# Optimization experiments

Measured on AMD Instinct MI355X. Metric: run time of the kernel, lower is better.

## Reference

```python
import jax, jax.numpy as jnp
import numpy as np

D_MODEL = 1024
NHEAD = 16
EPS = 1e-5


def pos_embed(x, pos):
    # Faithful, vectorized form of the sparse rotation matrix in the source.
    # Source builds rot[..., i, i+1] = sin(pos*i*omega) for even i and
    # rot[..., i, i-1] = cos(pos*i*omega) for odd i, then contracts the feature
    # dim of x against the rotation (intended einsum 'btf,btfd->btd').
    # Resulting column j: even j <- x[..., j+1]*cos(pos*(j+1)*omega),
    #                     odd  j <- x[..., j-1]*sin(pos*(j-1)*omega).
    d = x.shape[-1]
    omega = jnp.pi / d
    i_even = jnp.arange(0, d, 2, dtype=x.dtype)   # even rows -> odd output cols (sin)
    i_odd = jnp.arange(1, d, 2, dtype=x.dtype)    # odd rows  -> even output cols (cos)
    p = pos[..., None]  # (L,B,1)
    sin_part = jnp.sin(p * i_even * omega) * x[..., 0::2]  # -> odd columns
    cos_part = jnp.cos(p * i_odd * omega) * x[..., 1::2]   # -> even columns
    # interleave: even col = cos_part, odd col = sin_part
    return jnp.stack([cos_part, sin_part], axis=-1).reshape(x.shape)


def layer_norm_eps(x, w, b):
    # Source uses torch.var default (unbiased, ddof=1)
    mean = jnp.mean(x, axis=-1, keepdims=True)
    var = jnp.var(x, axis=-1, keepdims=True, ddof=1)
    return w * (x - mean) / jnp.sqrt(var + EPS) + b


def mha(q, k, v, w_qkv, b_qkv, w_o, b_o, nhead):
    L, B, E = q.shape
    S = k.shape[0]
    hd = E // nhead
    wq, wk, wv = jnp.split(w_qkv, 3, axis=0)
    bq, bk, bv = jnp.split(b_qkv, 3, axis=0)
    qp = (q @ wq.T + bq).reshape(L, B, nhead, hd).transpose(1, 2, 0, 3)  # (B,h,L,hd)
    kp = (k @ wk.T + bk).reshape(S, B, nhead, hd).transpose(1, 2, 0, 3)
    vp = (v @ wv.T + bv).reshape(S, B, nhead, hd).transpose(1, 2, 0, 3)
    scale = jnp.asarray(1.0 / np.sqrt(hd), q.dtype)
    scores = jnp.einsum('bhld,bhsd->bhls', qp, kp) * scale
    attn = jax.nn.softmax(scores, axis=-1)
    out = jnp.einsum('bhls,bhsd->bhld', attn, vp)
    out = out.transpose(2, 0, 1, 3).reshape(L, B, E) @ w_o.T + b_o
    ws = attn.mean(axis=1)  # average over heads, torch default
    return out, ws


def setup_inputs() -> dict:
    key = jax.random.key(0)
    ks = jax.random.split(key, 16)
    T, S, B, E, FF = 1024, 1024, 4, D_MODEL, 4096
    sd = 0.02
    return {
        'tgt': jax.random.normal(ks[0], (T, B, E), jnp.float32),
        'memory': jax.random.normal(ks[1], (S, B, E), jnp.float32),
        'pos': jax.random.uniform(ks[2], (S, B), jnp.float32) * S,
        'query_pos': jax.random.uniform(ks[3], (T, B), jnp.float32) * T,
        'w_qkv_self': jax.random.normal(ks[4], (3 * E, E), jnp.float32) * sd,
        'b_qkv_self': jnp.zeros((3 * E,), jnp.float32),
        'w_o_self': jax.random.normal(ks[5], (E, E), jnp.float32) * sd,
        'b_o_self': jnp.zeros((E,), jnp.float32),
        'w_qkv_cross': jax.random.normal(ks[6], (3 * E, E), jnp.float32) * sd,
        'b_qkv_cross': jnp.zeros((3 * E,), jnp.float32),
        'w_o_cross': jax.random.normal(ks[7], (E, E), jnp.float32) * sd,
        'b_o_cross': jnp.zeros((E,), jnp.float32),
        'w1': jax.random.normal(ks[8], (FF, E), jnp.float32) * sd,
        'b1': jnp.zeros((FF,), jnp.float32),
        'w2': jax.random.normal(ks[9], (E, FF), jnp.float32) * sd,
        'b2': jnp.zeros((E,), jnp.float32),
        'g1': jnp.ones((E,), jnp.float32),
        'beta1': jnp.zeros((E,), jnp.float32),
        'g2': jnp.ones((E,), jnp.float32),
        'beta2': jnp.zeros((E,), jnp.float32),
    }


def reference(tgt, memory, pos, query_pos,
              w_qkv_self, b_qkv_self, w_o_self, b_o_self,
              w_qkv_cross, b_qkv_cross, w_o_cross, b_o_cross,
              w1, b1, w2, b2, g1, beta1, g2, beta2):
    # normalize_before=False, residual=True, dropout inactive (eval)
    qk = pos_embed(tgt, query_pos)
    tgt2, _ = mha(qk, qk, tgt, w_qkv_self, b_qkv_self, w_o_self, b_o_self, NHEAD)
    tgt = tgt + tgt2
    tgt = layer_norm_eps(tgt, g1, beta1)
    tgt2, ws = mha(pos_embed(tgt, query_pos), pos_embed(memory, pos), memory,
                   w_qkv_cross, b_qkv_cross, w_o_cross, b_o_cross, NHEAD)
    tgt = tgt + tgt2
    tgt = layer_norm_eps(tgt, g2, beta2)
    tgt2 = jax.nn.relu(tgt @ w1.T + b1) @ w2.T + b2
    tgt = tgt + tgt2
    return tgt, ws
```

## Files before the change

kernel.cpp:

```cpp
#include <hip/hip_runtime.h>

typedef unsigned short u16;
typedef __attribute__((ext_vector_type(8))) short short8;
typedef __attribute__((ext_vector_type(8))) unsigned short u16x8;
typedef __attribute__((ext_vector_type(4))) float f32x4;

#define GLOAD16(SRC, DST) __builtin_amdgcn_global_load_lds( \
    (const __attribute__((address_space(1))) void*)(SRC),   \
    (__attribute__((address_space(3))) void*)(DST), 16, 0, 0)

#define SWZ(BKv, r) ((BKv) == 32 ? (((r) >> 1) & 3) : ((r) & 7))

#define QSCALE 0.18033688011112042f

__device__ __forceinline__ u16 f2bf(float f) {
  union { float f; unsigned u; } v; v.f = f;
  unsigned r = v.u + 0x7fffu + ((v.u >> 16) & 1u);
  return (u16)(r >> 16);
}
__device__ __forceinline__ float bf2f(u16 h) {
  union { unsigned u; float f; } v; v.u = ((unsigned)h) << 16;
  return v.f;
}

__global__ __launch_bounds__(256) void wcvt_kernel(const float* __restrict__ s0,
                                                   const float* __restrict__ s1,
                                                   const float* __restrict__ s2,
                                                   const float* __restrict__ s3,
                                                   const float* __restrict__ s4,
                                                   const float* __restrict__ s5,
                                                   u16* __restrict__ dst) {
  long i = ((long)blockIdx.x * 256 + threadIdx.x) * 4;
  const float* src; long off;
  if (i < 3145728)        { src = s0; off = 0; }
  else if (i < 4194304)   { src = s1; off = 3145728; }
  else if (i < 7340032)   { src = s2; off = 4194304; }
  else if (i < 8388608)   { src = s3; off = 7340032; }
  else if (i < 12582912)  { src = s4; off = 8388608; }
  else                    { src = s5; off = 12582912; }
  float4 v = *(const float4*)(src + (i - off));
  ushort4 o; o.x = f2bf(v.x); o.y = f2bf(v.y); o.z = f2bf(v.z); o.w = f2bf(v.w);
  *(ushort4*)(dst + i) = o;
}

__global__ __launch_bounds__(256) void pos_embed_kernel(const float* __restrict__ x,
                                                        const float* __restrict__ pos,
                                                        u16* __restrict__ out,
                                                        u16* __restrict__ out2,
                                                        u16* __restrict__ raw) {
  int m = blockIdx.x;
  int tid = threadIdx.x;
  float p = pos[m];
  long base = ((long)m << 10);
  int j = tid * 4;
  float4 xv = *(const float4*)(x + base + j);
  const float inv = 1.0f / 2048.0f;
  float r0 = p * (float)(j + 0) * inv;
  float r1 = p * (float)(j + 1) * inv;
  float r2 = p * (float)(j + 2) * inv;
  float r3 = p * (float)(j + 3) * inv;
  float s1 = __builtin_amdgcn_sinf(r0 - floorf(r0));
  float c0 = __builtin_amdgcn_cosf(r1 - floorf(r1));
  float s3 = __builtin_amdgcn_sinf(r2 - floorf(r2));
  float c2 = __builtin_amdgcn_cosf(r3 - floorf(r3));
  ushort4 o;
  o.x = f2bf(c0 * xv.y);
  o.y = f2bf(s1 * xv.x);
  o.z = f2bf(c2 * xv.w);
  o.w = f2bf(s3 * xv.z);
  *(ushort4*)(out + base + j) = o;
  if (out2) *(ushort4*)(out2 + base + j) = o;
  if (raw) {
    ushort4 rw; rw.x = f2bf(xv.x); rw.y = f2bf(xv.y); rw.z = f2bf(xv.z); rw.w = f2bf(xv.w);
    *(ushort4*)(raw + base + j) = rw;
  }
}

__global__ __launch_bounds__(256) void fattn_kernel(const u16* __restrict__ Q,
                                                    const u16* __restrict__ K,
                                                    const u16* __restrict__ Vt,
                                                    u16* __restrict__ AO,
                                                    float2* __restrict__ Ml) {
  __shared__ u16 lK[2][4096];
  __shared__ u16 lV[2][4096];
  __shared__ u16 lP[8][1024];
  const int tid = threadIdx.x, lane = tid & 63, wid = tid >> 6;
  const int nb = gridDim.x * gridDim.y;
  const int orig = blockIdx.y * gridDim.x + blockIdx.x;
  const int swz = (orig & 7) * (nb >> 3) + (orig >> 3);
  const int qt = swz & 7;
  const int bh = swz >> 3;
  const int b = bh >> 4, h = bh & 15;
  const u16* Qp = Q + ((long)bh << 16);
  const u16* Kp = K + ((long)bh << 16);
  const u16* Vp = Vt + ((long)bh << 16);
  const int q0 = qt << 7;
  const int cr = lane >> 4;

  short8 aAf0, aAf1, aBf0, aBf1;
  {
    const u16* qs = Qp + (long)(q0 + wid * 16 + (lane & 15)) * 64 + cr * 8;
    aAf0 = *(const short8*)qs;
    aAf1 = *(const short8*)(qs + 32);
    aBf0 = *(const short8*)(qs + 4096);
    aBf1 = *(const short8*)(qs + 4096 + 32);
  }

  float mA = -1e30f, lA_ = 0.f, mB = -1e30f, lB_ = 0.f;
  f32x4 accA[4] = {}, accB[4] = {};

  auto stage = [&](int bufi, int kv) {
    int s0 = kv << 6;
#pragma unroll
    for (int it = 0; it < 2; it++) {
      int c = it * 256 + tid;
      int row = c >> 3, ch = c & 7;
      int sch = (ch ^ (row & 7)) * 8;
      GLOAD16(Kp + (long)(s0 + row) * 64 + sch, &lK[bufi][c * 8]);
      GLOAD16(Vp + (long)row * 1024 + s0 + sch, &lV[bufi][c * 8]);
    }
  };

  stage(0, 0);
  __syncthreads();
  int buf = 0;
  for (int kv = 0; kv < 16; kv++) {
    if (kv < 15) stage(buf ^ 1, kv + 1);
    f32x4 sA[4], sB[4];
    __builtin_amdgcn_s_setprio(1);
#pragma unroll
    for (int j = 0; j < 4; j++) {
      int sr = j * 16 + (lane & 15);
      const short8 kf0 = *(const short8*)&lK[buf][sr * 64 + ((cr ^ (sr & 7)) * 8)];
      const short8 kf1 = *(const short8*)&lK[buf][sr * 64 + (((4 + cr) ^ (sr & 7)) * 8)];
      f32x4 zA = {}, zB = {};
      zA = __builtin_amdgcn_mfma_f32_16x16x32_bf16(kf0, aAf0, zA, 0, 0, 0);
      zB = __builtin_amdgcn_mfma_f32_16x16x32_bf16(kf0, aBf0, zB, 0, 0, 0);
      sA[j] = __builtin_amdgcn_mfma_f32_16x16x32_bf16(kf1, aAf1, zA, 0, 0, 0);
      sB[j] = __builtin_amdgcn_mfma_f32_16x16x32_bf16(kf1, aBf1, zB, 0, 0, 0);
    }
    __builtin_amdgcn_s_setprio(0);
    {
      float tm = fmaxf(fmaxf(fmaxf(sA[0][0], sA[0][1]), fmaxf(sA[0][2], sA[0][3])),
                       fmaxf(fmaxf(sA[1][0], sA[1][1]), fmaxf(sA[1][2], sA[1][3])));
      float t2 = fmaxf(fmaxf(fmaxf(sA[2][0], sA[2][1]), fmaxf(sA[2][2], sA[2][3])),
                       fmaxf(fmaxf(sA[3][0], sA[3][1]), fmaxf(sA[3][2], sA[3][3])));
      tm = fmaxf(tm, t2);
      tm = fmaxf(tm, __shfl_xor(tm, 16));
      tm = fmaxf(tm, __shfl_xor(tm, 32));
      if (!__all(tm - mA <= 8.0f)) {
        float mn = fmaxf(mA, tm);
        float f = __builtin_amdgcn_exp2f(mA - mn);
        mA = mn; lA_ *= f;
#pragma unroll
        for (int r = 0; r < 4; r++) {
          float fr = __shfl(f, cr * 4 + r);
          accA[0][r] *= fr; accA[1][r] *= fr; accA[2][r] *= fr; accA[3][r] *= fr;
        }
      }
      float rs = 0.f;
#pragma unroll
      for (int j = 0; j < 4; j++)
#pragma unroll
        for (int r = 0; r < 4; r++) {
          float p = __builtin_amdgcn_exp2f(sA[j][r] - mA);
          sA[j][r] = p;
          rs += p;
        }
      rs += __shfl_xor(rs, 16);
      rs += __shfl_xor(rs, 32);
      lA_ += rs;
    }
    {
      float tm = fmaxf(fmaxf(fmaxf(sB[0][0], sB[0][1]), fmaxf(sB[0][2], sB[0][3])),
                       fmaxf(fmaxf(sB[1][0], sB[1][1]), fmaxf(sB[1][2], sB[1][3])));
      float t2 = fmaxf(fmaxf(fmaxf(sB[2][0], sB[2][1]), fmaxf(sB[2][2], sB[2][3])),
                       fmaxf(fmaxf(sB[3][0], sB[3][1]), fmaxf(sB[3][2], sB[3][3])));
      tm = fmaxf(tm, t2);
      tm = fmaxf(tm, __shfl_xor(tm, 16));
      tm = fmaxf(tm, __shfl_xor(tm, 32));
      if (!__all(tm - mB <= 8.0f)) {
        float mn = fmaxf(mB, tm);
        float f = __builtin_amdgcn_exp2f(mB - mn);
        mB = mn; lB_ *= f;
#pragma unroll
        for (int r = 0; r < 4; r++) {
          float fr = __shfl(f, cr * 4 + r);
          accB[0][r] *= fr; accB[1][r] *= fr; accB[2][r] *= fr; accB[3][r] *= fr;
        }
      }
      float rs = 0.f;
#pragma unroll
      for (int j = 0; j < 4; j++)
#pragma unroll
        for (int r = 0; r < 4; r++) {
          float p = __builtin_amdgcn_exp2f(sB[j][r] - mB);
          sB[j][r] = p;
          rs += p;
        }
      rs += __shfl_xor(rs, 16);
      rs += __shfl_xor(rs, 32);
      lB_ += rs;
    }
    {
      int q = lane & 15;
      int rowoff = q * 64;
      int qs7 = q & 7;
      u16* pwA = lP[wid];
      u16* pwB = lP[4 + wid];
#pragma unroll
      for (int j = 0; j < 4; j++) {
        int chunk = 2 * j + (cr >> 1);
        int idx = rowoff + ((chunk ^ qs7) * 8) + 4 * (cr & 1);
        uint2 pkA, pkB;
        asm("v_cvt_pk_bf16_f32 %0, %1, %2"
            : "=v"(pkA.x) : "v"(sA[j][0]), "v"(sA[j][1]));
        asm("v_cvt_pk_bf16_f32 %0, %1, %2"
            : "=v"(pkA.y) : "v"(sA[j][2]), "v"(sA[j][3]));
        asm("v_cvt_pk_bf16_f32 %0, %1, %2"
            : "=v"(pkB.x) : "v"(sB[j][0]), "v"(sB[j][1]));
        asm("v_cvt_pk_bf16_f32 %0, %1, %2"
            : "=v"(pkB.y) : "v"(sB[j][2]), "v"(sB[j][3]));
        *(uint2*)(pwA + idx) = pkA;
        *(uint2*)(pwB + idx) = pkB;
      }
    }
    {
      int ql = lane & 15;
      const u16* prA = &lP[wid][ql * 64];
      const u16* prB = &lP[4 + wid][ql * 64];
      short8 paA0 = *(const short8*)&prA[(cr ^ (ql & 7)) * 8];
      short8 paA1 = *(const short8*)&prA[((4 + cr) ^ (ql & 7)) * 8];
      short8 paB0 = *(const short8*)&prB[(cr ^ (ql & 7)) * 8];
      short8 paB1 = *(const short8*)&prB[((4 + cr) ^ (ql & 7)) * 8];
      __builtin_amdgcn_s_setprio(1);
#pragma unroll
      for (int j = 0; j < 4; j++) {
        int dr = j * 16 + (lane & 15);
        const short8 vf0 = *(const short8*)&lV[buf][dr * 64 + ((cr ^ (dr & 7)) * 8)];
        const short8 vf1 = *(const short8*)&lV[buf][dr * 64 + (((4 + cr) ^ (dr & 7)) * 8)];
        accA[j] = __builtin_amdgcn_mfma_f32_16x16x32_bf16(paA0, vf0, accA[j], 0, 0, 0);
        accB[j] = __builtin_amdgcn_mfma_f32_16x16x32_bf16(paB0, vf0, accB[j], 0, 0, 0);
        accA[j] = __builtin_amdgcn_mfma_f32_16x16x32_bf16(paA1, vf1, accA[j], 0, 0, 0);
        accB[j] = __builtin_amdgcn_mfma_f32_16x16x32_bf16(paB1, vf1, accB[j], 0, 0, 0);
      }
      __builtin_amdgcn_s_setprio(0);
    }
    __syncthreads();
    buf ^= 1;
  }
  float invA = 1.0f / lA_, invB = 1.0f / lB_;
  float iA[4], iB[4];
#pragma unroll
  for (int r = 0; r < 4; r++) {
    iA[r] = __shfl(invA, cr * 4 + r);
    iB[r] = __shfl(invB, cr * 4 + r);
  }
  const int ecol = (b << 10) + (h << 6);
#pragma unroll
  for (int j = 0; j < 4; j++)
#pragma unroll
    for (int r = 0; r < 4; r++) {
      int t = q0 + wid * 16 + cr * 4 + r;
      int e = ecol + j * 16 + (lane & 15);
      AO[(long)t * 4096 + e] = f2bf(accA[j][r] * iA[r]);
      AO[(long)(t + 64) * 4096 + e] = f2bf(accB[j][r] * iB[r]);
    }
  if (Ml && lane < 16) {
    int t = q0 + wid * 16 + lane;
    Ml[((long)bh << 10) + t] = make_float2(mA, invA);
    Ml[((long)bh << 10) + t + 64] = make_float2(mB, invB);
  }
}

__global__ __launch_bounds__(256) void wsrec_kernel(const u16* __restrict__ Q,
                                                    const u16* __restrict__ K,
                                                    const float2* __restrict__ Ml,
                                                    float* __restrict__ ws) {
  __shared__ u16 lK[2][4096];
  const int tid = threadIdx.x, lane = tid & 63, wid = tid >> 6;
  const int nb = gridDim.x * gridDim.y;
  const int orig = blockIdx.y * gridDim.x + blockIdx.x;
  const int swz = (orig & 7) * (nb >> 3) + (orig >> 3);
  const int st = swz & 15, lt = swz >> 4;
  const int b = blockIdx.z;
  const int s0 = st << 6, l0 = lt << 6;
  const int cr = lane >> 4;

  auto stage = [&](int bufi, int h) {
    const u16* Kp = K + (((long)(b * 16 + h)) << 16);
#pragma unroll
    for (int it = 0; it < 2; it++) {
      int c = it * 256 + tid;
      int row = c >> 3, ch = c & 7;
      GLOAD16(Kp + (long)(s0 + row) * 64 + ((ch ^ (row & 7)) * 8), &lK[bufi][c * 8]);
    }
  };

  f32x4 wacc[4] = {};
  stage(0, 0);
  __syncthreads();
  int buf = 0;
  for (int h = 0; h < 16; h++) {
    if (h < 15) stage(buf ^ 1, h + 1);
    const int bh = b * 16 + h;
    short8 af0, af1;
    {
      const u16* qs = Q + ((long)bh << 16) + (long)(l0 + wid * 16 + (lane & 15)) * 64 + cr * 8;
      af0 = *(const short8*)qs;
      af1 = *(const short8*)(qs + 32);
    }
    f32x4 accs[4];
    __builtin_amdgcn_s_setprio(1);
#pragma unroll
    for (int j = 0; j < 4; j++) {
      int sr = j * 16 + (lane & 15);
      const short8 kf0 = *(const short8*)&lK[buf][sr * 64 + ((cr ^ (sr & 7)) * 8)];
      const short8 kf1 = *(const short8*)&lK[buf][sr * 64 + (((4 + cr) ^ (sr & 7)) * 8)];
      f32x4 zz = {};
      zz = __builtin_amdgcn_mfma_f32_16x16x32_bf16(af0, kf0, zz, 0, 0, 0);
      accs[j] = __builtin_amdgcn_mfma_f32_16x16x32_bf16(af1, kf1, zz, 0, 0, 0);
    }
    __builtin_amdgcn_s_setprio(0);
    float mm[4], il[4];
#pragma unroll
    for (int r = 0; r < 4; r++) {
      float2 v = Ml[((long)bh << 10) + l0 + wid * 16 + (lane >> 4) * 4 + r];
      mm[r] = v.x; il[r] = v.y * 0.0625f;
    }
#pragma unroll
    for (int j = 0; j < 4; j++)
#pragma unroll
      for (int r = 0; r < 4; r++)
        wacc[j][r] += __builtin_amdgcn_exp2f(accs[j][r] - mm[r]) * il[r];
    __syncthreads();
    buf ^= 1;
  }
#pragma unroll
  for (int j = 0; j < 4; j++)
#pragma unroll
    for (int r = 0; r < 4; r++) {
      int li = l0 + wid * 16 + (lane >> 4) * 4 + r;
      int si = s0 + j * 16 + (lane & 15);
      ws[((long)b << 20) + (long)li * 1024 + si] = wacc[j][r];
    }
}

__global__ __launch_bounds__(256) void ln_kernel(const float* __restrict__ X,
                                                 const float* __restrict__ D1,
                                                 const float* __restrict__ D2,
                                                 const float* __restrict__ bo,
                                                 const float* __restrict__ g,
                                                 const float* __restrict__ be,
                                                 float* __restrict__ out,
                                                 u16* __restrict__ bfout,
                                                 const float* __restrict__ pepos) {
  int mrow = blockIdx.x;
  int tid = threadIdx.x, lane = tid & 63, wid = tid >> 6;
  long base = ((long)mrow << 10);
  float4 a = *(const float4*)(X + base + tid * 4);
  float4 b = *(const float4*)(D1 + base + tid * 4);
  float x0 = a.x + b.x, x1 = a.y + b.y, x2 = a.z + b.z, x3 = a.w + b.w;
  if (D2) {
    float4 c = *(const float4*)(D2 + base + tid * 4);
    x0 += c.x; x1 += c.y; x2 += c.z; x3 += c.w;
  }
  if (bo) {
    float4 c = *(const float4*)(bo + tid * 4);
    x0 += c.x; x1 += c.y; x2 += c.z; x3 += c.w;
  }
  float s = x0 + x1 + x2 + x3;
#pragma unroll
  for (int o = 32; o; o >>= 1) s += __shfl_xor(s, o);
  __shared__ float red[4];
  if (lane == 0) red[wid] = s;
  __syncthreads();
  float mean = (red[0] + red[1] + red[2] + red[3]) * (1.0f / 1024.0f);
  float d0 = x0 - mean, d1 = x1 - mean, d2 = x2 - mean, d3 = x3 - mean;
  float ss = d0 * d0 + d1 * d1 + d2 * d2 + d3 * d3;
#pragma unroll
  for (int o = 32; o; o >>= 1) ss += __shfl_xor(ss, o);
  __syncthreads();
  if (lane == 0) red[wid] = ss;
  __syncthreads();
  float var = (red[0] + red[1] + red[2] + red[3]) * (1.0f / 1023.0f);
  float sc = 1.0f / sqrtf(var + 1e-5f);
  float4 gv = *(const float4*)(g + tid * 4);
  float4 bv = *(const float4*)(be + tid * 4);
  float y0 = gv.x * d0 * sc + bv.x;
  float y1 = gv.y * d1 * sc + bv.y;
  float y2 = gv.z * d2 * sc + bv.z;
  float y3 = gv.w * d3 * sc + bv.w;
  float4 o4; o4.x = y0; o4.y = y1; o4.z = y2; o4.w = y3;
  *(float4*)(out + base + tid * 4) = o4;
  if (bfout) {
    ushort4 hh;
    if (pepos) {
      float p = pepos[mrow];
      int j = tid * 4;
      const float inv = 1.0f / 2048.0f;
      float r0 = p * (float)(j + 0) * inv;
      float r1 = p * (float)(j + 1) * inv;
      float r2 = p * (float)(j + 2) * inv;
      float r3 = p * (float)(j + 3) * inv;
      float s1 = __builtin_amdgcn_sinf(r0 - floorf(r0));
      float c0 = __builtin_amdgcn_cosf(r1 - floorf(r1));
      float s3 = __builtin_amdgcn_sinf(r2 - floorf(r2));
      float c2 = __builtin_amdgcn_cosf(r3 - floorf(r3));
      hh.x = f2bf(c0 * y1);
      hh.y = f2bf(s1 * y0);
      hh.z = f2bf(c2 * y3);
      hh.w = f2bf(s3 * y2);
    } else {
      hh.x = f2bf(y0); hh.y = f2bf(y1); hh.z = f2bf(y2); hh.w = f2bf(y3);
    }
    *(ushort4*)(bfout + base + tid * 4) = hh;
  }
}

__global__ __launch_bounds__(256) void add3_kernel(const float* __restrict__ X,
                                                   const float* __restrict__ P0,
                                                   const float* __restrict__ P1,
                                                   const float* __restrict__ b,
                                                   float* __restrict__ out) {
  long i = ((long)blockIdx.x * 256 + threadIdx.x) * 4;
  int col = (int)(i & 1023);
  float4 x = *(const float4*)(X + i);
  float4 p = *(const float4*)(P0 + i);
  float4 q = *(const float4*)(P1 + i);
  float4 bb = *(const float4*)(b + col);
  float4 o;
  o.x = x.x + p.x + q.x + bb.x;
  o.y = x.y + p.y + q.y + bb.y;
  o.z = x.z + p.z + q.z + bb.z;
  o.w = x.w + p.w + q.w + bb.w;
  *(float4*)(out + i) = o;
}

template <int BM, int BN, int BK, int WR, int WC, int NT, int DB>
__global__ __launch_bounds__(NT)
void gemm_bt_kernel(const u16* __restrict__ A, const u16* __restrict__ B,
                    void* __restrict__ C, const float* __restrict__ bias,
                    int lda, int ldb, int ldc, int K,
                    long sAz, long sBz, long sCz, long sbz,
                    float alpha, int flags) {
  constexpr int WTM = BM / WR, WTN = BN / WC;
  constexpr int FM = WTM / 16, FN = WTN / 16;
  constexpr int NC = BK / 8;
  __shared__ u16 lA[DB][BM * BK];
  __shared__ u16 lB[DB][BN * BK];
  const int tid = threadIdx.x, lane = tid & 63, wid = tid >> 6;
  const int wr = wid / WC, wc = wid % WC;
  const int z = blockIdx.z;

  const int nwg = gridDim.x * gridDim.y;
  const int orig = blockIdx.y * gridDim.x + blockIdx.x;
  const int qq = nwg >> 3, rr = nwg & 7;
  const int xcd = orig & 7, idx = orig >> 3;
  const int swz = (xcd < rr ? xcd * (qq + 1) : rr * (qq + 1) + (xcd - rr) * qq) + idx;
  const int bxs = swz % gridDim.x;
  const int bys = swz / gridDim.x;

  const u16* Ab = A + z * sAz + (long)bys * BM * lda;
  const u16* Bb = B + z * sBz + (long)bxs * BN * ldb;

  f32x4 acc[FM][FN] = {};

  auto stage = [&](int bufi, int k0) {
#pragma unroll
    for (int c0 = 0; c0 < BM * NC; c0 += NT) {
      int c = c0 + tid;
      if ((BM * NC) % NT == 0 || c < BM * NC) {
        int row = c / NC, ch = c % NC;
        int sch = ch ^ SWZ(BK, row);
        GLOAD16(Ab + (long)row * lda + k0 + sch * 8, &lA[bufi][c * 8]);
      }
    }
#pragma unroll
    for (int c0 = 0; c0 < BN * NC; c0 += NT) {
      int c = c0 + tid;
      if ((BN * NC) % NT == 0 || c < BN * NC) {
        int row = c / NC, ch = c % NC;
        int sch = ch ^ SWZ(BK, row);
        GLOAD16(Bb + (long)row * ldb + k0 + sch * 8, &lB[bufi][c * 8]);
      }
    }
  };

  auto compute = [&](int bufi) {
#pragma unroll
    for (int kk = 0; kk < BK / 32; kk++) {
      short8 afv[FM], bfv[FN];
#pragma unroll
      for (int i = 0; i < FM; i++) {
        int row = wr * WTM + i * 16 + (lane & 15);
        int ch = kk * 4 + (lane >> 4);
        afv[i] = *(const short8*)&lA[bufi][row * BK + ((ch ^ SWZ(BK, row)) * 8)];
      }
#pragma unroll
      for (int j = 0; j < FN; j++) {
        int row = wc * WTN + j * 16 + (lane & 15);
        int ch = kk * 4 + (lane >> 4);
        bfv[j] = *(const short8*)&lB[bufi][row * BK + ((ch ^ SWZ(BK, row)) * 8)];
      }
#pragma unroll
      for (int i = 0; i < FM; i++)
#pragma unroll
        for (int j = 0; j < FN; j++)
          acc[i][j] = __builtin_amdgcn_mfma_f32_16x16x32_bf16(afv[i], bfv[j], acc[i][j], 0, 0, 0);
    }
  };

  const int nk = K / BK;
  stage(0, 0);
  __syncthreads();
  int cur = 0;
  for (int t = 0; t < nk; t++) {
    if (t + 1 < nk) stage(cur ^ 1, (t + 1) * BK);
    compute(cur);
    __syncthreads();
    cur ^= 1;
  }

  const long rbase = (long)bys * BM + wr * WTM;
  const int cbase = bxs * BN + wc * WTN;
  const float* bz = bias ? (bias + z * sbz) : nullptr;
#pragma unroll
  for (int i = 0; i < FM; i++)
#pragma unroll
    for (int j = 0; j < FN; j++)
#pragma unroll
      for (int r = 0; r < 4; r++) {
        long row = rbase + i * 16 + ((lane >> 4) * 4 + r);
        int col = cbase + j * 16 + (lane & 15);
        float v = acc[i][j][r];
        if (!(flags & 8)) v *= alpha;
        if (flags & 1) v += bz[col];
        if ((flags & 8) && z == 0) v *= alpha;
        if (flags & 2) v = fmaxf(v, 0.0f);
        if (flags & 16) {
          int t = (int)(row >> 2), bb = (int)(row & 3);
          int hh = col >> 6, dd = col & 63;
          long base16 = ((long)(bb * 16 + hh)) << 16;
          long off = (long)z * 4194304 + base16 +
                     (z == 2 ? (long)dd * 1024 + t : (long)t * 64 + dd);
          ((u16*)C)[off] = f2bf(v);
        } else {
          long off = (long)z * sCz + row * (long)ldc + col;
          if (flags & 4) ((float*)C)[off] = v;
          else ((u16*)C)[off] = f2bf(v);
        }
      }
}

extern "C" void kernel_launch(void* const* d_in, const int* in_sizes, int n_in,
                              void* d_out, int out_size, void* d_ws, size_t ws_size,
                              hipStream_t stream) {
  const float* tgt  = (const float*)d_in[0];
  const float* mem  = (const float*)d_in[1];
  const float* pos  = (const float*)d_in[2];
  const float* qpos = (const float*)d_in[3];
  const float* wqkvS = (const float*)d_in[4];
  const float* bqkvS = (const float*)d_in[5];
  const float* woS   = (const float*)d_in[6];
  const float* boS   = (const float*)d_in[7];
  const float* wqkvC = (const float*)d_in[8];
  const float* bqkvC = (const float*)d_in[9];
  const float* woC   = (const float*)d_in[10];
  const float* boC   = (const float*)d_in[11];
  const float* w1  = (const float*)d_in[12];
  const float* b1  = (const float*)d_in[13];
  const float* w2  = (const float*)d_in[14];
  const float* b2  = (const float*)d_in[15];
  const float* g1  = (const float*)d_in[16];
  const float* be1 = (const float*)d_in[17];
  const float* g2  = (const float*)d_in[18];
  const float* be2 = (const float*)d_in[19];

  const size_t MB = 1024ull * 1024ull;
  float* out0 = (float*)d_out;
  float* wsout = out0 + 4194304;

  char* W = (char*)d_ws;
  u16* wb = (u16*)W;
  u16* wqkvS_b = wb;
  u16* woS_b   = wb + 3145728;
  u16* wqkvC_b = wb + 4194304;
  u16* woC_b   = wb + 7340032;
  u16* w1_b    = wb + 8388608;
  u16* w2_b    = wb + 12582912;
  float* Xf   = (float*)(W + 32 * MB);
  float* OPar = (float*)(W + 48 * MB);
  u16* bf1 = (u16*)(W + 80 * MB);
  u16* bf2 = (u16*)(W + 88 * MB);
  u16* bf3 = (u16*)(W + 96 * MB);
  float2* Ml = (float2*)(W + 96 * MB);
  u16* Qb  = (u16*)(W + 104 * MB);
  u16* Kb  = (u16*)(W + 112 * MB);
  u16* Vtb = (u16*)(W + 120 * MB);
  u16* AOb = (u16*)(W + 128 * MB);
  u16* F1  = (u16*)(W + 104 * MB);

  wcvt_kernel<<<16384, 256, 0, stream>>>(wqkvS, woS, wqkvC, woC, w1, w2, wb);

  pos_embed_kernel<<<4096, 256, 0, stream>>>(tgt, qpos, bf1, bf2, bf3);
  gemm_bt_kernel<128, 128, 32, 2, 4, 512, 2><<<dim3(8, 32, 3), 512, 0, stream>>>(
      bf1, wqkvS_b, Qb, bqkvS, 1024, 1024, 0, 1024,
      4194304, 1048576, 0, 1024, QSCALE, 1 | 8 | 16);
  fattn_kernel<<<dim3(8, 64), 256, 0, stream>>>(Qb, Kb, Vtb, AOb, nullptr);
  gemm_bt_kernel<128, 128, 32, 2, 4, 512, 2><<<dim3(8, 32, 2), 512, 0, stream>>>(
      AOb, woS_b, OPar, nullptr, 1024, 1024, 1024, 512,
      512, 512, 4194304, 0, 1.0f, 4);
  ln_kernel<<<4096, 256, 0, stream>>>(tgt, OPar, OPar + 4194304, boS, g1, be1,
                                      Xf, bf1, qpos);

  pos_embed_kernel<<<4096, 256, 0, stream>>>(mem, pos, bf2, nullptr, bf3);
  gemm_bt_kernel<128, 128, 32, 2, 4, 512, 2><<<dim3(8, 32, 3), 512, 0, stream>>>(
      bf1, wqkvC_b, Qb, bqkvC, 1024, 1024, 0, 1024,
      4194304, 1048576, 0, 1024, QSCALE, 1 | 8 | 16);
  fattn_kernel<<<dim3(8, 64), 256, 0, stream>>>(Qb, Kb, Vtb, AOb, Ml);
  wsrec_kernel<<<dim3(16, 16, 4), 256, 0, stream>>>(Qb, Kb, Ml, wsout);
  gemm_bt_kernel<128, 128, 32, 2, 4, 512, 2><<<dim3(8, 32, 2), 512, 0, stream>>>(
      AOb, woC_b, OPar, nullptr, 1024, 1024, 1024, 512,
      512, 512, 4194304, 0, 1.0f, 4);
  ln_kernel<<<4096, 256, 0, stream>>>(Xf, OPar, OPar + 4194304, boC, g2, be2,
                                      Xf, bf1, nullptr);

  gemm_bt_kernel<128, 128, 32, 2, 4, 512, 2><<<dim3(32, 32, 1), 512, 0, stream>>>(
      bf1, w1_b, F1, b1, 1024, 1024, 4096, 1024, 0, 0, 0, 0, 1.0f, 1 | 2);
  gemm_bt_kernel<128, 128, 32, 2, 4, 512, 2><<<dim3(8, 32, 2), 512, 0, stream>>>(
      F1, w2_b, OPar, nullptr, 4096, 4096, 1024, 2048,
      2048, 2048, 4194304, 0, 1.0f, 4);
  add3_kernel<<<4096, 256, 0, stream>>>(Xf, OPar, OPar + 4194304, b2, out0);
}
```

Measured before the change: 404.9 us.

## Write V row-major from QKV GEMM, transpose separately, and tile-group block swizzle

The QKV projection epilogue used to write V directly in transposed layout with strided 2-byte stores; now V is written row-major and a new shared-memory transpose kernel produces the transposed layout before attention. The GEMM block mapping is also changed to group blocks into 8-wide column tiles within each XCD chunk, aiming at better L2 reuse. A new flag lets the z=1 (K) slice reuse the same A input as Q, so pos_embed no longer writes a duplicate buffer. This adds two extra kernel launches and an extra V round trip through memory.

New measurement: 415.7 us. 2.7% more time.

```diff
diff --git a/kernel.cpp b/kernel.cpp
--- a/kernel.cpp
+++ b/kernel.cpp
@@ -74,6 +74,29 @@
     ushort4 rw; rw.x = f2bf(xv.x); rw.y = f2bf(xv.y); rw.z = f2bf(xv.z); rw.w = f2bf(xv.w);
     *(ushort4*)(raw + base + j) = rw;
   }
+}
+
+__global__ __launch_bounds__(256) void vtrans_kernel(const u16* __restrict__ Vrow,
+                                                     u16* __restrict__ Vtb) {
+  __shared__ u16 tile[64][65];
+  int bh = blockIdx.x, tc = blockIdx.y;
+  int b = bh >> 4, h = bh & 15;
+  int t0 = tc << 6;
+  int tid = threadIdx.x;
+  int tl = tid >> 2, dc = tid & 3;
+  const u16* src = Vrow + ((long)(t0 + tl) * 4 + b) * 1024 + h * 64 + dc * 16;
+  u16x8 v0 = *(const u16x8*)src;
+  u16x8 v1 = *(const u16x8*)(src + 8);
+#pragma unroll
+  for (int k = 0; k < 8; k++) { tile[tl][dc * 16 + k] = v0[k]; tile[tl][dc * 16 + 8 + k] = v1[k]; }
+  __syncthreads();
+  int dl = tid >> 2, t4 = tid & 3;
+  u16x8 o0, o1;
+#pragma unroll
+  for (int k = 0; k < 8; k++) { o0[k] = tile[t4 * 16 + k][dl]; o1[k] = tile[t4 * 16 + 8 + k][dl]; }
+  u16* dst = Vtb + ((long)bh << 16) + (long)dl * 1024 + t0 + t4 * 16;
+  *(u16x8*)dst = o0;
+  *(u16x8*)(dst + 8) = o1;
 }
 
 __global__ __launch_bounds__(256) void fattn_kernel(const u16* __restrict__ Q,
@@ -458,10 +481,24 @@
   const int qq = nwg >> 3, rr = nwg & 7;
   const int xcd = orig & 7, idx = orig >> 3;
   const int swz = (xcd < rr ? xcd * (qq + 1) : rr * (qq + 1) + (xcd - rr) * qq) + idx;
-  const int bxs = swz % gridDim.x;
-  const int bys = swz / gridDim.x;
-
-  const u16* Ab = A + z * sAz + (long)bys * BM * lda;
+  int bxs, bys;
+  if ((nwg & 7) == 0 && (gridDim.x & 7) == 0) {
+    const int CS = qq;
+    const int rows = CS / gridDim.x;
+    const int chunk0 = (swz / CS) * CS;
+    int cs = swz - chunk0;
+    int tile = cs / (rows * 8);
+    int w = cs % (rows * 8);
+    bxs = tile * 8 + (w & 7);
+    bys = chunk0 / gridDim.x + w / 8;
+  } else {
+    bxs = swz % gridDim.x;
+    bys = swz / gridDim.x;
+  }
+
+  long azo = (long)z * sAz;
+  if ((flags & 32) && z == 1) azo = 0;
+  const u16* Ab = A + azo + (long)bys * BM * lda;
   const u16* Bb = B + z * sBz + (long)bxs * BN * ldb;
 
   f32x4 acc[FM][FN] = {};
@@ -539,12 +576,15 @@
         if ((flags & 8) && z == 0) v *= alpha;
         if (flags & 2) v = fmaxf(v, 0.0f);
         if (flags & 16) {
-          int t = (int)(row >> 2), bb = (int)(row & 3);
-          int hh = col >> 6, dd = col & 63;
-          long base16 = ((long)(bb * 16 + hh)) << 16;
-          long off = (long)z * 4194304 + base16 +
-                     (z == 2 ? (long)dd * 1024 + t : (long)t * 64 + dd);
-          ((u16*)C)[off] = f2bf(v);
+          if (z == 2) {
+            ((u16*)C)[12582912 + row * 1024 + col] = f2bf(v);
+          } else {
+            int t = (int)(row >> 2), bb = (int)(row & 3);
+            int hh = col >> 6, dd = col & 63;
+            long base16 = ((long)(bb * 16 + hh)) << 16;
+            long off = (long)z * 4194304 + base16 + (long)t * 64 + dd;
+            ((u16*)C)[off] = f2bf(v);
+          }
         } else {
           long off = (long)z * sCz + row * (long)ldc + col;
           if (flags & 4) ((float*)C)[off] = v;
@@ -598,15 +638,17 @@
   u16* Qb  = (u16*)(W + 104 * MB);
   u16* Kb  = (u16*)(W + 112 * MB);
   u16* Vtb = (u16*)(W + 120 * MB);
+  u16* Vrow = (u16*)(W + 128 * MB);
   u16* AOb = (u16*)(W + 128 * MB);
   u16* F1  = (u16*)(W + 104 * MB);
 
   wcvt_kernel<<<16384, 256, 0, stream>>>(wqkvS, woS, wqkvC, woC, w1, w2, wb);
 
-  pos_embed_kernel<<<4096, 256, 0, stream>>>(tgt, qpos, bf1, bf2, bf3);
+  pos_embed_kernel<<<4096, 256, 0, stream>>>(tgt, qpos, bf1, nullptr, bf3);
   gemm_bt_kernel<128, 128, 32, 2, 4, 512, 2><<<dim3(8, 32, 3), 512, 0, stream>>>(
       bf1, wqkvS_b, Qb, bqkvS, 1024, 1024, 0, 1024,
-      4194304, 1048576, 0, 1024, QSCALE, 1 | 8 | 16);
+      4194304, 1048576, 0, 1024, QSCALE, 1 | 8 | 16 | 32);
+  vtrans_kernel<<<dim3(64, 16), 256, 0, stream>>>(Vrow, Vtb);
   fattn_kernel<<<dim3(8, 64), 256, 0, stream>>>(Qb, Kb, Vtb, AOb, nullptr);
   gemm_bt_kernel<128, 128, 32, 2, 4, 512, 2><<<dim3(8, 32, 2), 512, 0, stream>>>(
       AOb, woS_b, OPar, nullptr, 1024, 1024, 1024, 512,
@@ -618,6 +660,7 @@
   gemm_bt_kernel<128, 128, 32, 2, 4, 512, 2><<<dim3(8, 32, 3), 512, 0, stream>>>(
       bf1, wqkvC_b, Qb, bqkvC, 1024, 1024, 0, 1024,
       4194304, 1048576, 0, 1024, QSCALE, 1 | 8 | 16);
+  vtrans_kernel<<<dim3(64, 16), 256, 0, stream>>>(Vrow, Vtb);
   fattn_kernel<<<dim3(8, 64), 256, 0, stream>>>(Qb, Kb, Vtb, AOb, Ml);
   wsrec_kernel<<<dim3(16, 16, 4), 256, 0, stream>>>(Qb, Kb, Ml, wsout);
   gemm_bt_kernel<128, 128, 32, 2, 4, 512, 2><<<dim3(8, 32, 2), 512, 0, stream>>>(
```
